# Performance work log

Hardware: AMD Instinct MI355X
Metric: run time of the kernel (lower is better)

The kernel has to match this reference:

```python
import jax, jax.numpy as jnp
import numpy as np

N_EMBED = 1024
HEAD_SIZE = 64
BLOCK_SIZE = 4096


def setup_inputs() -> dict:
    key = jax.random.key(0)
    ks = jax.random.split(key, 7)
    s = 1.0 / np.sqrt(N_EMBED)
    return {
        "batch_x": jax.random.normal(ks[0], (4, 4096, N_EMBED), dtype=jnp.float32),
        "Wk": jax.random.uniform(ks[1], (N_EMBED, HEAD_SIZE), jnp.float32, -s, s),
        "bk": jax.random.uniform(ks[2], (HEAD_SIZE,), jnp.float32, -s, s),
        "Wq": jax.random.uniform(ks[3], (N_EMBED, HEAD_SIZE), jnp.float32, -s, s),
        "bq": jax.random.uniform(ks[4], (HEAD_SIZE,), jnp.float32, -s, s),
        "Wv": jax.random.uniform(ks[5], (N_EMBED, HEAD_SIZE), jnp.float32, -s, s),
        "bv": jax.random.uniform(ks[6], (HEAD_SIZE,), jnp.float32, -s, s),
    }


def reference(batch_x, Wk, bk, Wq, bq, Wv, bv):
    # batch_x: [B, T, C]
    T = batch_x.shape[1]
    keys = batch_x @ Wk + bk      # [B, T, H]
    queries = batch_x @ Wq + bq   # [B, T, H]
    values = batch_x @ Wv + bv    # [B, T, H]
    scale = 1.0 / jnp.sqrt(jnp.asarray(HEAD_SIZE, batch_x.dtype))
    wei = jnp.einsum("bqh,bkh->bqk", queries, keys) * scale  # [B, T, T]
    causal = jnp.tril(jnp.ones((T, T), dtype=bool))
    wei = jnp.where(causal, wei, -jnp.inf)
    wei = jax.nn.softmax(wei, axis=-1)
    out = jnp.einsum("bqk,bkh->bqh", wei, values)  # [B, T, H]
    return out
```

## Files before the change

### kernel.cpp

```cpp
#include <hip/hip_runtime.h>


using bf16x8 = __attribute__((ext_vector_type(8))) short;
using bf16x4 = __attribute__((ext_vector_type(4))) short;
using f32x4  = __attribute__((ext_vector_type(4))) float;

#define QSCALE 0.1803368867f

__device__ __forceinline__ unsigned short f2bf(float f) {
  union { float f; unsigned int u; } v; v.f = f;
  unsigned int r = v.u + 0x7fffu + ((v.u >> 16) & 1u);
  return (unsigned short)(r >> 16);
}

__device__ __forceinline__ float fexp2(float x) {
#if __has_builtin(__builtin_amdgcn_exp2f)
  return __builtin_amdgcn_exp2f(x);
#else
  float r; asm("v_exp_f32 %0, %1" : "=v"(r) : "v"(x)); return r;
#endif
}

__device__ __forceinline__ void gl_lds16(const void* g, void* l) {
  __builtin_amdgcn_global_load_lds(
      (const __attribute__((address_space(1))) void*)g,
      (__attribute__((address_space(3))) void*)l, 16, 0, 0);
}

__device__ __forceinline__ f32x4 mfma16(bf16x4 a, bf16x4 b, f32x4 c) {
#if __has_builtin(__builtin_amdgcn_mfma_f32_16x16x16bf16_1k)
  return __builtin_amdgcn_mfma_f32_16x16x16bf16_1k(a, b, c, 0, 0, 0);
#else
  f32x4 d;
  asm volatile("v_mfma_f32_16x16x16_bf16 %0, %1, %2, %3"
               : "=v"(d) : "v"(a), "v"(b), "v"(c));
  return d;
#endif
}

__global__ __launch_bounds__(512) void proj6_kernel(
    const float* __restrict__ X,  const float* __restrict__ Wk,
    const float* __restrict__ Wq, const float* __restrict__ Wv,
    const float* __restrict__ bk, const float* __restrict__ bq,
    const float* __restrict__ bv, unsigned short* __restrict__ Kr,
    unsigned short* __restrict__ Qs, unsigned short* __restrict__ Vt) {
  __shared__ __align__(16) unsigned short Xl[32 * 72];
  __shared__ __align__(16) unsigned short Wl[192 * 72];
  const int tid = threadIdx.x;
  const int m0  = blockIdx.x * 32;
  const int w   = tid >> 6;
  const int mt  = w & 1;
  const int nh  = w >> 1;
  const int ln  = tid & 63;
  const int l15 = ln & 15;
  const int l4  = ln >> 4;
  const int wn  = tid & 63;
  const int wk8 = (tid >> 6) * 8;
  const int xr  = tid >> 4, xc = tid & 15;
  const f32x4 zero4 = {0.f, 0.f, 0.f, 0.f};

  f32x4 acc[3];
  #pragma unroll
  for (int i = 0; i < 3; ++i) acc[i] = zero4;

  float4 xp = *reinterpret_cast<const float4*>(X + (size_t)(m0 + xr) * 1024 + xc * 4);

  for (int kb = 0; kb < 16; ++kb) {
    __syncthreads();
    bf16x4 o;
    o[0] = (short)f2bf(xp.x); o[1] = (short)f2bf(xp.y);
    o[2] = (short)f2bf(xp.z); o[3] = (short)f2bf(xp.w);
    *reinterpret_cast<bf16x4*>(&Xl[xr * 72 + xc * 4]) = o;
    if (kb < 15) {
      xp = *reinterpret_cast<const float4*>(
          X + (size_t)(m0 + xr) * 1024 + (kb + 1) * 64 + xc * 4);
    }
    #pragma unroll
    for (int c = 0; c < 3; ++c) {
      const float* Wsrc = (c == 0) ? Wk : ((c == 1) ? Wq : Wv);
      bf16x8 w0;
      #pragma unroll
      for (int j = 0; j < 8; ++j)
        w0[j] = (short)f2bf(Wsrc[(size_t)(kb * 64 + wk8 + j) * 64 + wn]);
      *reinterpret_cast<bf16x8*>(&Wl[(c * 64 + wn) * 72 + wk8]) = w0;
    }
    __syncthreads();
    bf16x8 a0 = *reinterpret_cast<const bf16x8*>(&Xl[(mt * 16 + l15) * 72 + l4 * 8]);
    bf16x8 a1 = *reinterpret_cast<const bf16x8*>(&Xl[(mt * 16 + l15) * 72 + 32 + l4 * 8]);
    #pragma unroll
    for (int i = 0; i < 3; ++i) {
      int row = nh * 48 + i * 16 + l15;
      bf16x8 b0 = *reinterpret_cast<const bf16x8*>(&Wl[row * 72 + l4 * 8]);
      bf16x8 b1 = *reinterpret_cast<const bf16x8*>(&Wl[row * 72 + 32 + l4 * 8]);
      acc[i] = __builtin_amdgcn_mfma_f32_16x16x32_bf16(a0, b0, acc[i], 0, 0, 0);
      acc[i] = __builtin_amdgcn_mfma_f32_16x16x32_bf16(a1, b1, acc[i], 0, 0, 0);
    }
  }
  #pragma unroll
  for (int i = 0; i < 3; ++i) {
    int j = nh * 48 + i * 16 + l15;
    int mr0 = m0 + mt * 16 + l4 * 4;
    if (j < 64) {
      #pragma unroll
      for (int r = 0; r < 4; ++r)
        Kr[(size_t)(mr0 + r) * 64 + j] = f2bf(acc[i][r] + bk[j]);
    } else if (j < 128) {
      int jq = j - 64;
      #pragma unroll
      for (int r = 0; r < 4; ++r)
        Qs[(size_t)(mr0 + r) * 64 + jq] = f2bf((acc[i][r] + bq[jq]) * QSCALE);
    } else {
      int h = j - 128;
      int bb = mr0 >> 12, t0 = mr0 & 4095;
      ushort4 o;
      o.x = f2bf(acc[i][0] + bv[h]); o.y = f2bf(acc[i][1] + bv[h]);
      o.z = f2bf(acc[i][2] + bv[h]); o.w = f2bf(acc[i][3] + bv[h]);
      *reinterpret_cast<ushort4*>(&Vt[((size_t)(bb * 64 + h)) * 4096 + t0]) = o;
    }
  }
}

__global__ __launch_bounds__(512) void attn8_kernel(
    const unsigned short* __restrict__ Qs,
    const unsigned short* __restrict__ Kr,
    const unsigned short* __restrict__ Vt,
    float* __restrict__ out) {
  __shared__ __align__(16) char smem[98304];
  const int tid = threadIdx.x;
  const int w   = tid >> 6;
  const int ln  = tid & 63;
  const int l15 = ln & 15;
  const int l4  = ln >> 4;
  const int bid = blockIdx.x;
  const int pr  = bid >> 2;
  const int b   = bid & 3;
  const f32x4 zero4 = {0.f, 0.f, 0.f, 0.f};

  char* Kl = smem + w * 12288;
  char* Vl = Kl + 8192;

  const int kLane = (ln >> 3) * 128 + ((ln & 7) ^ (ln >> 3)) * 16;
  const int vLane = (ln >> 2) * 8192 + (((ln & 3) ^ ((ln >> 3) & 3))) * 16;
  const char* Kbase = (const char*)Kr + (size_t)b * 4096 * 128;
  const char* Vbase = (const char*)Vt + (size_t)b * 64 * 8192;

  auto phase = [&](int qt, bool entryBar) {
    if (entryBar) __syncthreads();
    const int qbase  = qt * 32;
    const int ntiles = qt + 1;

    const unsigned short* Q0 = Qs + ((size_t)b * 4096 + qbase + l15) * 64;
    const bf16x8 qa0 = *reinterpret_cast<const bf16x8*>(Q0 + l4 * 8);
    const bf16x8 qa1 = *reinterpret_cast<const bf16x8*>(Q0 + 32 + l4 * 8);
    const bf16x8 qb0 = *reinterpret_cast<const bf16x8*>(Q0 + 1024 + l4 * 8);
    const bf16x8 qb1 = *reinterpret_cast<const bf16x8*>(Q0 + 1024 + 32 + l4 * 8);

    f32x4 accA[4], accB[4];
    #pragma unroll
    for (int i = 0; i < 4; ++i) { accA[i] = zero4; accB[i] = zero4; }
    float mA = -1e30f, lA = 0.f, mB = -1e30f, lB = 0.f;

    auto stageK = [&](int buf, int t) {
      const char* src = Kbase + (size_t)t * 4096;
      char* dst = Kl + buf * 4096;
      #pragma unroll
      for (int c = 0; c < 4; ++c)
        gl_lds16(src + c * 1024 + kLane, dst + c * 1024 + ln * 16);
    };
    auto stageV = [&](int t) {
      const char* src = Vbase + (size_t)t * 64;
      #pragma unroll
      for (int c = 0; c < 4; ++c)
        gl_lds16(src + (size_t)c * 16 * 8192 + vLane, Vl + c * 1024 + ln * 16);
    };

    int cur = 0;
    if (w < ntiles) stageK(0, w);

    for (int t = w; t < ntiles; t += 8) {
      stageV(t);
      const bool hn = (t + 8 < ntiles);
      if (hn) stageK(cur ^ 1, t + 8);

      if (hn) asm volatile("s_waitcnt vmcnt(8)" ::: "memory");
      else    asm volatile("s_waitcnt vmcnt(4)" ::: "memory");
      __builtin_amdgcn_sched_barrier(0);

      f32x4 sA[2], sB[2];
      #pragma unroll
      for (int i = 0; i < 2; ++i) { sA[i] = zero4; sB[i] = zero4; }
      __builtin_amdgcn_s_setprio(1);
      #pragma unroll
      for (int nt = 0; nt < 2; ++nt) {
        const int krow = nt * 16 + l15;
        const unsigned short* kp =
            (const unsigned short*)(Kl + cur * 4096) + krow * 64;
        bf16x8 k0 = *reinterpret_cast<const bf16x8*>(kp + ((l4 ^ (krow & 7)) << 3));
        bf16x8 k1 = *reinterpret_cast<const bf16x8*>(kp + (((l4 + 4) ^ (krow & 7)) << 3));
        sA[nt] = __builtin_amdgcn_mfma_f32_16x16x32_bf16(k0, qa0, sA[nt], 0, 0, 0);
        sA[nt] = __builtin_amdgcn_mfma_f32_16x16x32_bf16(k1, qa1, sA[nt], 0, 0, 0);
        sB[nt] = __builtin_amdgcn_mfma_f32_16x16x32_bf16(k0, qb0, sB[nt], 0, 0, 0);
        sB[nt] = __builtin_amdgcn_mfma_f32_16x16x32_bf16(k1, qb1, sB[nt], 0, 0, 0);
      }
      __builtin_amdgcn_s_setprio(0);

      if (t == ntiles - 1) {
        const int qm = qbase + l15 - t * 32;
        #pragma unroll
        for (int nt = 0; nt < 2; ++nt)
          #pragma unroll
          for (int r = 0; r < 4; ++r) {
            int kvl = nt * 16 + 4 * l4 + r;
            if (kvl > qm)      sA[nt][r] = -1e30f;
            if (kvl > qm + 16) sB[nt][r] = -1e30f;
          }
      }

      bf16x4 paA[2], paB[2];
      {
        float x0 = fmaxf(fmaxf(sA[0][0], sA[0][1]), fmaxf(sA[0][2], sA[0][3]));
        float x1 = fmaxf(fmaxf(sA[1][0], sA[1][1]), fmaxf(sA[1][2], sA[1][3]));
        float xm = fmaxf(x0, x1);
        xm = fmaxf(xm, __shfl_xor(xm, 16));
        xm = fmaxf(xm, __shfl_xor(xm, 32));
        float mn = fmaxf(mA, xm);
        float cc = fexp2(mA - mn);
        mA = mn; lA *= cc;
        #pragma unroll
        for (int ht = 0; ht < 4; ++ht)
          #pragma unroll
          for (int r = 0; r < 4; ++r) accA[ht][r] *= cc;
        float sum = 0.f;
        #pragma unroll
        for (int nt = 0; nt < 2; ++nt) {
          #pragma unroll
          for (int r = 0; r < 4; ++r) {
            float p = fexp2(sA[nt][r] - mA);
            sA[nt][r] = p;
            paA[nt][r] = (short)f2bf(p);
          }
          sum += (sA[nt][0] + sA[nt][1]) + (sA[nt][2] + sA[nt][3]);
        }
        sum += __shfl_xor(sum, 16);
        sum += __shfl_xor(sum, 32);
        lA += sum;
      }
      {
        float x0 = fmaxf(fmaxf(sB[0][0], sB[0][1]), fmaxf(sB[0][2], sB[0][3]));
        float x1 = fmaxf(fmaxf(sB[1][0], sB[1][1]), fmaxf(sB[1][2], sB[1][3]));
        float xm = fmaxf(x0, x1);
        xm = fmaxf(xm, __shfl_xor(xm, 16));
        xm = fmaxf(xm, __shfl_xor(xm, 32));
        float mn = fmaxf(mB, xm);
        float cc = fexp2(mB - mn);
        mB = mn; lB *= cc;
        #pragma unroll
        for (int ht = 0; ht < 4; ++ht)
          #pragma unroll
          for (int r = 0; r < 4; ++r) accB[ht][r] *= cc;
        float sum = 0.f;
        #pragma unroll
        for (int nt = 0; nt < 2; ++nt) {
          #pragma unroll
          for (int r = 0; r < 4; ++r) {
            float p = fexp2(sB[nt][r] - mB);
            sB[nt][r] = p;
            paB[nt][r] = (short)f2bf(p);
          }
          sum += (sB[nt][0] + sB[nt][1]) + (sB[nt][2] + sB[nt][3]);
        }
        sum += __shfl_xor(sum, 16);
        sum += __shfl_xor(sum, 32);
        lB += sum;
      }

      if (hn) asm volatile("s_waitcnt vmcnt(4)" ::: "memory");
      else    asm volatile("s_waitcnt vmcnt(0)" ::: "memory");
      __builtin_amdgcn_sched_barrier(0);

      __builtin_amdgcn_s_setprio(1);
      #pragma unroll
      for (int nt = 0; nt < 2; ++nt) {
        #pragma unroll
        for (int ht = 0; ht < 4; ++ht) {
          const int vrow = ht * 16 + l15;
          const int g16 = (nt * 2 + (l4 >> 1)) ^ ((vrow >> 1) & 3);
          const char* vp = Vl + vrow * 64 + (g16 << 4) + ((l4 & 1) << 3);
          bf16x4 vf = *reinterpret_cast<const bf16x4*>(vp);
          accA[ht] = mfma16(vf, paA[nt], accA[ht]);
          accB[ht] = mfma16(vf, paB[nt], accB[ht]);
        }
      }
      __builtin_amdgcn_s_setprio(0);
      cur ^= 1;
    }

    __syncthreads();
    float* MO = (float*)smem;
    float* ML = (float*)(smem + 8 * 2 * 16 * 68 * 4);
    #pragma unroll
    for (int ht = 0; ht < 4; ++ht) {
      *reinterpret_cast<f32x4*>(&MO[((w * 2 + 0) * 16 + l15) * 68 + ht * 16 + 4 * l4]) = accA[ht];
      *reinterpret_cast<f32x4*>(&MO[((w * 2 + 1) * 16 + l15) * 68 + ht * 16 + 4 * l4]) = accB[ht];
    }
    if (l4 == 0) {
      ML[((w * 2 + 0) * 2 + 0) * 16 + l15] = mA;
      ML[((w * 2 + 0) * 2 + 1) * 16 + l15] = lA;
      ML[((w * 2 + 1) * 2 + 0) * 16 + l15] = mB;
      ML[((w * 2 + 1) * 2 + 1) * 16 + l15] = lB;
    }
    __syncthreads();
    {
      const int hf = tid >> 8;
      const int q  = (tid >> 4) & 15;
      const int hq = tid & 15;
      float mv[8], lv[8];
      float mM = -1e30f;
      #pragma unroll
      for (int p = 0; p < 8; ++p) {
        mv[p] = ML[((p * 2 + hf) * 2 + 0) * 16 + q];
        lv[p] = ML[((p * 2 + hf) * 2 + 1) * 16 + q];
        mM = fmaxf(mM, mv[p]);
      }
      float lT = 0.f, a[8];
      #pragma unroll
      for (int p = 0; p < 8; ++p) { a[p] = fexp2(mv[p] - mM); lT += lv[p] * a[p]; }
      float linv = 1.0f / lT;
      f32x4 o = zero4;
      #pragma unroll
      for (int p = 0; p < 8; ++p) {
        f32x4 v = *reinterpret_cast<const f32x4*>(
            &MO[((p * 2 + hf) * 16 + q) * 68 + hq * 4]);
        o[0] += v[0] * a[p]; o[1] += v[1] * a[p];
        o[2] += v[2] * a[p]; o[3] += v[3] * a[p];
      }
      float4 ov;
      ov.x = o[0] * linv; ov.y = o[1] * linv;
      ov.z = o[2] * linv; ov.w = o[3] * linv;
      *reinterpret_cast<float4*>(
          out + ((size_t)b * 4096 + qbase + hf * 16 + q) * 64 + hq * 4) = ov;
    }
  };

  phase(127 - pr, false);
  phase(pr, true);
}

template <bool WRITE_Q>
__global__ __launch_bounds__(256) void proj_kernel(
    const float* __restrict__ X,  const float* __restrict__ Wk,
    const float* __restrict__ Wq, const float* __restrict__ Wv,
    const float* __restrict__ bk, const float* __restrict__ bq,
    const float* __restrict__ bv, unsigned short* __restrict__ Kr,
    unsigned short* __restrict__ Qs, unsigned short* __restrict__ Vt) {
  constexpr int NT = WRITE_Q ? 12 : 8;
  constexpr int NC = NT / 4;
  __shared__ __align__(16) unsigned short Xl[64 * 72];
  __shared__ __align__(16) unsigned short Wl[NT * 16 * 72];
  const int tid = threadIdx.x;
  const int m0  = blockIdx.x * 64;
  const int w   = tid >> 6;
  const int ln  = tid & 63;
  const int l15 = ln & 15;
  const int l4  = ln >> 4;
  const f32x4 zero4 = {0.f, 0.f, 0.f, 0.f};
  f32x4 acc[NT];
  #pragma unroll
  for (int i = 0; i < NT; ++i) acc[i] = zero4;
  const int wn = tid & 63;
  const int wk = (tid >> 6) * 16;
  for (int kb = 0; kb < 16; ++kb) {
    __syncthreads();
    #pragma unroll
    for (int p = 0; p < 4; ++p) {
      int chunk = tid + p * 256;
      int r = chunk >> 4, c4 = chunk & 15;
      const float4 xv = *reinterpret_cast<const float4*>(
          X + (size_t)(m0 + r) * 1024 + kb * 64 + c4 * 4);
      bf16x4 o;
      o[0] = (short)f2bf(xv.x); o[1] = (short)f2bf(xv.y);
      o[2] = (short)f2bf(xv.z); o[3] = (short)f2bf(xv.w);
      *reinterpret_cast<bf16x4*>(&Xl[r * 72 + c4 * 4]) = o;
    }
    #pragma unroll
    for (int c = 0; c < NC; ++c) {
      const float* Wsrc = (c == 0) ? Wk : ((WRITE_Q && c == 1) ? Wq : Wv);
      bf16x8 w0, w1;
      #pragma unroll
      for (int j = 0; j < 8; ++j)
        w0[j] = (short)f2bf(Wsrc[(size_t)(kb * 64 + wk + j) * 64 + wn]);
      #pragma unroll
      for (int j = 0; j < 8; ++j)
        w1[j] = (short)f2bf(Wsrc[(size_t)(kb * 64 + wk + 8 + j) * 64 + wn]);
      *reinterpret_cast<bf16x8*>(&Wl[(c * 64 + wn) * 72 + wk])     = w0;
      *reinterpret_cast<bf16x8*>(&Wl[(c * 64 + wn) * 72 + wk + 8]) = w1;
    }
    __syncthreads();
    bf16x8 a0 = *reinterpret_cast<const bf16x8*>(&Xl[(w * 16 + l15) * 72 + l4 * 8]);
    bf16x8 a1 = *reinterpret_cast<const bf16x8*>(&Xl[(w * 16 + l15) * 72 + 32 + l4 * 8]);
    #pragma unroll
    for (int nt = 0; nt < NT; ++nt) {
      bf16x8 b0 = *reinterpret_cast<const bf16x8*>(&Wl[(nt * 16 + l15) * 72 + l4 * 8]);
      bf16x8 b1 = *reinterpret_cast<const bf16x8*>(&Wl[(nt * 16 + l15) * 72 + 32 + l4 * 8]);
      acc[nt] = __builtin_amdgcn_mfma_f32_16x16x32_bf16(a0, b0, acc[nt], 0, 0, 0);
      acc[nt] = __builtin_amdgcn_mfma_f32_16x16x32_bf16(a1, b1, acc[nt], 0, 0, 0);
    }
  }
  #pragma unroll
  for (int nt = 0; nt < NT; ++nt) {
    int j = nt * 16 + l15;
    #pragma unroll
    for (int r = 0; r < 4; ++r) {
      int m = m0 + w * 16 + l4 * 4 + r;
      float v = acc[nt][r];
      if (nt < 4) {
        Kr[(size_t)m * 64 + j] = f2bf(v + bk[j]);
      } else if (WRITE_Q && nt < 8) {
        Qs[(size_t)m * 64 + (j - 64)] = f2bf((v + bq[j - 64]) * QSCALE);
      } else {
        int h = j - (WRITE_Q ? 128 : 64);
        int bb = m >> 12, t = m & 4095;
        Vt[((size_t)(bb * 64 + h)) * 4096 + t] = f2bf(v + bv[h]);
      }
    }
  }
}

__global__ __launch_bounds__(256) void attnB_kernel(
    const unsigned short* __restrict__ Kr,
    const unsigned short* __restrict__ Vt,
    const float* __restrict__ X, const float* __restrict__ Wq,
    const float* __restrict__ bq, float* __restrict__ out) {
  __shared__ __align__(16) unsigned short Kl[64 * 72];
  __shared__ __align__(16) unsigned short Vl[64 * 72];
  __shared__ __align__(16) unsigned short Pl[4 * 16 * 72];
  const int tid = threadIdx.x;
  const int w   = tid >> 6;
  const int ln  = tid & 63;
  const int l15 = ln & 15;
  const int l4  = ln >> 4;
  const int b   = blockIdx.y;
  const int q0  = blockIdx.x * 64;
  const int qrow = q0 + w * 16;
  const f32x4 zero4 = {0.f, 0.f, 0.f, 0.f};
  unsigned short* Pw = &Pl[w * 16 * 72];
  f32x4 accq[4];
  #pragma unroll
  for (int i = 0; i < 4; ++i) accq[i] = zero4;
  const int wn = tid & 63;
  const int wk = (tid >> 6) * 16;
  for (int kb = 0; kb < 16; ++kb) {
    __syncthreads();
    #pragma unroll
    for (int p = 0; p < 4; ++p) {
      int chunk = tid + p * 256;
      int r = chunk >> 4, c4 = chunk & 15;
      const float4 xv = *reinterpret_cast<const float4*>(
          X + ((size_t)b * 4096 + q0 + r) * 1024 + kb * 64 + c4 * 4);
      bf16x4 o;
      o[0] = (short)f2bf(xv.x); o[1] = (short)f2bf(xv.y);
      o[2] = (short)f2bf(xv.z); o[3] = (short)f2bf(xv.w);
      *reinterpret_cast<bf16x4*>(&Kl[r * 72 + c4 * 4]) = o;
    }
    bf16x8 w0, w1;
    #pragma unroll
    for (int j = 0; j < 8; ++j)
      w0[j] = (short)f2bf(Wq[(size_t)(kb * 64 + wk + j) * 64 + wn]);
    #pragma unroll
    for (int j = 0; j < 8; ++j)
      w1[j] = (short)f2bf(Wq[(size_t)(kb * 64 + wk + 8 + j) * 64 + wn]);
    *reinterpret_cast<bf16x8*>(&Vl[wn * 72 + wk])     = w0;
    *reinterpret_cast<bf16x8*>(&Vl[wn * 72 + wk + 8]) = w1;
    __syncthreads();
    bf16x8 a0 = *reinterpret_cast<const bf16x8*>(&Kl[(w * 16 + l15) * 72 + l4 * 8]);
    bf16x8 a1 = *reinterpret_cast<const bf16x8*>(&Kl[(w * 16 + l15) * 72 + 32 + l4 * 8]);
    #pragma unroll
    for (int nt = 0; nt < 4; ++nt) {
      bf16x8 b0 = *reinterpret_cast<const bf16x8*>(&Vl[(nt * 16 + l15) * 72 + l4 * 8]);
      bf16x8 b1 = *reinterpret_cast<const bf16x8*>(&Vl[(nt * 16 + l15) * 72 + 32 + l4 * 8]);
      accq[nt] = __builtin_amdgcn_mfma_f32_16x16x32_bf16(a0, b0, accq[nt], 0, 0, 0);
      accq[nt] = __builtin_amdgcn_mfma_f32_16x16x32_bf16(a1, b1, accq[nt], 0, 0, 0);
    }
  }
  #pragma unroll
  for (int nt = 0; nt < 4; ++nt) {
    int h = nt * 16 + l15;
    #pragma unroll
    for (int r = 0; r < 4; ++r)
      Pw[(l4 * 4 + r) * 72 + h] = f2bf((accq[nt][r] + bq[h]) * 0.125f);
  }
  asm volatile("s_waitcnt lgkmcnt(0)" ::: "memory");
  __builtin_amdgcn_sched_barrier(0);
  bf16x8 qa0 = *reinterpret_cast<const bf16x8*>(&Pw[l15 * 72 + l4 * 8]);
  bf16x8 qa1 = *reinterpret_cast<const bf16x8*>(&Pw[l15 * 72 + 32 + l4 * 8]);
  f32x4 acco[4];
  #pragma unroll
  for (int i = 0; i < 4; ++i) acco[i] = zero4;
  float mrow[4] = {-1e30f, -1e30f, -1e30f, -1e30f};
  float lrow[4] = {0.f, 0.f, 0.f, 0.f};
  const int ktmax = blockIdx.x;
  for (int kt = 0; kt <= ktmax; ++kt) {
    const int kv0 = kt * 64;
    __syncthreads();
    #pragma unroll
    for (int p = 0; p < 2; ++p) {
      int chunk = tid + p * 256;
      int r = chunk >> 3, c8 = chunk & 7;
      *reinterpret_cast<bf16x8*>(&Kl[r * 72 + c8 * 8]) =
          *reinterpret_cast<const bf16x8*>(Kr + ((size_t)b * 4096 + kv0 + r) * 64 + c8 * 8);
      *reinterpret_cast<bf16x8*>(&Vl[r * 72 + c8 * 8]) =
          *reinterpret_cast<const bf16x8*>(Vt + ((size_t)b * 64 + r) * 4096 + kv0 + c8 * 8);
    }
    __syncthreads();
    f32x4 s[4];
    #pragma unroll
    for (int i = 0; i < 4; ++i) s[i] = zero4;
    #pragma unroll
    for (int nt = 0; nt < 4; ++nt) {
      bf16x8 k0 = *reinterpret_cast<const bf16x8*>(&Kl[(nt * 16 + l15) * 72 + l4 * 8]);
      bf16x8 k1 = *reinterpret_cast<const bf16x8*>(&Kl[(nt * 16 + l15) * 72 + 32 + l4 * 8]);
      s[nt] = __builtin_amdgcn_mfma_f32_16x16x32_bf16(qa0, k0, s[nt], 0, 0, 0);
      s[nt] = __builtin_amdgcn_mfma_f32_16x16x32_bf16(qa1, k1, s[nt], 0, 0, 0);
    }
    if (kt == ktmax) {
      #pragma unroll
      for (int nt = 0; nt < 4; ++nt) {
        int kv_g = kv0 + nt * 16 + l15;
        #pragma unroll
        for (int r = 0; r < 4; ++r) {
          int q_g = qrow + l4 * 4 + r;
          if (kv_g > q_g) s[nt][r] = -1e30f;
        }
      }
    }
    #pragma unroll
    for (int r = 0; r < 4; ++r) {
      float t = fmaxf(fmaxf(s[0][r], s[1][r]), fmaxf(s[2][r], s[3][r]));
      t = fmaxf(t, __shfl_xor(t, 1));
      t = fmaxf(t, __shfl_xor(t, 2));
      t = fmaxf(t, __shfl_xor(t, 4));
      t = fmaxf(t, __shfl_xor(t, 8));
      float mnew = fmaxf(mrow[r], t);
      float cc = __expf(mrow[r] - mnew);
      mrow[r] = mnew;
      lrow[r] *= cc;
      acco[0][r] *= cc; acco[1][r] *= cc; acco[2][r] *= cc; acco[3][r] *= cc;
    }
    #pragma unroll
    for (int nt = 0; nt < 4; ++nt) {
      #pragma unroll
      for (int r = 0; r < 4; ++r) {
        float p = __expf(s[nt][r] - mrow[r]);
        s[nt][r] = p;
        Pw[(l4 * 4 + r) * 72 + nt * 16 + l15] = f2bf(p);
      }
    }
    #pragma unroll
    for (int r = 0; r < 4; ++r) {
      float t = s[0][r] + s[1][r] + s[2][r] + s[3][r];
      t += __shfl_xor(t, 1);
      t += __shfl_xor(t, 2);
      t += __shfl_xor(t, 4);
      t += __shfl_xor(t, 8);
      lrow[r] += t;
    }
    asm volatile("s_waitcnt lgkmcnt(0)" ::: "memory");
    __builtin_amdgcn_sched_barrier(0);
    #pragma unroll
    for (int ks = 0; ks < 2; ++ks) {
      bf16x8 pa = *reinterpret_cast<const bf16x8*>(&Pw[l15 * 72 + ks * 32 + l4 * 8]);
      #pragma unroll
      for (int ht = 0; ht < 4; ++ht) {
        bf16x8 vf = *reinterpret_cast<const bf16x8*>(&Vl[(ht * 16 + l15) * 72 + ks * 32 + l4 * 8]);
        acco[ht] = __builtin_amdgcn_mfma_f32_16x16x32_bf16(pa, vf, acco[ht], 0, 0, 0);
      }
    }
  }
  float* ob = out + ((size_t)b * 4096 + qrow) * 64;
  #pragma unroll
  for (int ht = 0; ht < 4; ++ht) {
    #pragma unroll
    for (int r = 0; r < 4; ++r) {
      ob[(l4 * 4 + r) * 64 + ht * 16 + l15] = acco[ht][r] / lrow[r];
    }
  }
}

extern "C" void kernel_launch(void* const* d_in, const int* in_sizes, int n_in,
                              void* d_out, int out_size, void* d_ws, size_t ws_size,
                              hipStream_t stream) {
  const float* X  = (const float*)d_in[0];
  const float* Wk = (const float*)d_in[1];
  const float* bk = (const float*)d_in[2];
  const float* Wq = (const float*)d_in[3];
  const float* bq = (const float*)d_in[4];
  const float* Wv = (const float*)d_in[5];
  const float* bv = (const float*)d_in[6];
  float* out = (float*)d_out;

  char* ws = (char*)d_ws;
  const size_t SZ = 2097152;
  unsigned short* Kr = (unsigned short*)(ws);
  unsigned short* Vt = (unsigned short*)(ws + SZ);

  if (ws_size >= 3 * SZ) {
    unsigned short* Qs = (unsigned short*)(ws + 2 * SZ);
    proj6_kernel<<<512, 512, 0, stream>>>(X, Wk, Wq, Wv, bk, bq, bv, Kr, Qs, Vt);
    attn8_kernel<<<256, 512, 0, stream>>>(Qs, Kr, Vt, out);
  } else {
    proj_kernel<false><<<256, 256, 0, stream>>>(X, Wk, Wq, Wv, bk, bq, bv, Kr, nullptr, Vt);
    attnB_kernel<<<dim3(64, 4), 256, 0, stream>>>(Kr, Vt, X, Wq, bq, out);
  }
}
```

Before: 61.31 us.

## Pre-transpose weights to bf16 and double-buffer projection loads via direct-to-LDS

Adds a small pre-kernel that converts Wk/Wq/Wv to a transposed bf16 layout once per call. This removes the strided fp32 weight gathers and conversions that every projection block used to repeat. The projection kernel now stages X (as fp32) and the weights straight into XOR-swizzled, double-buffered LDS using global_load_lds, converting X to bf16 at read time. That overlaps the next tile's loads with the MFMAs and halves the barriers. The cost is an extra kernel launch, double the LDS footprint, and fp32 X in LDS. If the workspace is too small it falls back to borrowing the output buffer for scratch.

```diff
diff --git a/kernel.cpp b/kernel.cpp
--- a/kernel.cpp
+++ b/kernel.cpp
@@ -38,14 +38,26 @@
 #endif
 }
 
-__global__ __launch_bounds__(512) void proj6_kernel(
-    const float* __restrict__ X,  const float* __restrict__ Wk,
-    const float* __restrict__ Wq, const float* __restrict__ Wv,
+__global__ __launch_bounds__(256) void prep_w_kernel(
+    const float* __restrict__ Wk, const float* __restrict__ Wq,
+    const float* __restrict__ Wv, unsigned short* __restrict__ Wt) {
+  int j = blockIdx.x;
+  const float* src = (j < 64) ? Wk : ((j < 128) ? Wq : Wv);
+  int jj = j & 63;
+  #pragma unroll
+  for (int p = 0; p < 4; ++p) {
+    int k = threadIdx.x + p * 256;
+    Wt[j * 1024 + k] = f2bf(src[k * 64 + jj]);
+  }
+}
+
+__global__ __launch_bounds__(512) void proj8_kernel(
+    const float* __restrict__ X, const unsigned short* __restrict__ Wt,
     const float* __restrict__ bk, const float* __restrict__ bq,
     const float* __restrict__ bv, unsigned short* __restrict__ Kr,
     unsigned short* __restrict__ Qs, unsigned short* __restrict__ Vt) {
-  __shared__ __align__(16) unsigned short Xl[32 * 72];
-  __shared__ __align__(16) unsigned short Wl[192 * 72];
+  __shared__ __align__(16) float          Xl[2][32 * 64];
+  __shared__ __align__(16) unsigned short Wl[2][192 * 64];
   const int tid = threadIdx.x;
   const int m0  = blockIdx.x * 32;
   const int w   = tid >> 6;
@@ -54,48 +66,66 @@
   const int ln  = tid & 63;
   const int l15 = ln & 15;
   const int l4  = ln >> 4;
-  const int wn  = tid & 63;
-  const int wk8 = (tid >> 6) * 8;
-  const int xr  = tid >> 4, xc = tid & 15;
   const f32x4 zero4 = {0.f, 0.f, 0.f, 0.f};
 
+  const int xr = tid >> 4, xc = tid & 15;
+  const size_t xsrcLane = (size_t)(m0 + xr) * 4096 + ((xc ^ (xr & 7)) << 4);
+  const char* Xb = (const char*)X;
+  const char* Wb = (const char*)Wt;
+
   f32x4 acc[3];
   #pragma unroll
   for (int i = 0; i < 3; ++i) acc[i] = zero4;
 
-  float4 xp = *reinterpret_cast<const float4*>(X + (size_t)(m0 + xr) * 1024 + xc * 4);
-
+  auto stageX = [&](int buf, int kb) {
+    gl_lds16(Xb + xsrcLane + kb * 256, (char*)&Xl[buf][0] + tid * 16);
+  };
+  auto stageW = [&](int buf, int kb) {
+    #pragma unroll
+    for (int s = 0; s < 3; ++s) {
+      int g = tid + s * 512;
+      int row = g >> 3, gc = g & 7;
+      gl_lds16(Wb + (size_t)row * 2048 + kb * 128 + ((gc ^ (row & 7)) << 4),
+               (char*)&Wl[buf][0] + g * 16);
+    }
+  };
+
+  stageX(0, 0);
+  stageW(0, 0);
+  asm volatile("s_waitcnt vmcnt(0)" ::: "memory");
+  __syncthreads();
+
+  const int rr = mt * 16 + l15;
+  const int rs7 = rr & 7;
   for (int kb = 0; kb < 16; ++kb) {
-    __syncthreads();
-    bf16x4 o;
-    o[0] = (short)f2bf(xp.x); o[1] = (short)f2bf(xp.y);
-    o[2] = (short)f2bf(xp.z); o[3] = (short)f2bf(xp.w);
-    *reinterpret_cast<bf16x4*>(&Xl[xr * 72 + xc * 4]) = o;
-    if (kb < 15) {
-      xp = *reinterpret_cast<const float4*>(
-          X + (size_t)(m0 + xr) * 1024 + (kb + 1) * 64 + xc * 4);
-    }
-    #pragma unroll
-    for (int c = 0; c < 3; ++c) {
-      const float* Wsrc = (c == 0) ? Wk : ((c == 1) ? Wq : Wv);
-      bf16x8 w0;
-      #pragma unroll
-      for (int j = 0; j < 8; ++j)
-        w0[j] = (short)f2bf(Wsrc[(size_t)(kb * 64 + wk8 + j) * 64 + wn]);
-      *reinterpret_cast<bf16x8*>(&Wl[(c * 64 + wn) * 72 + wk8]) = w0;
-    }
-    __syncthreads();
-    bf16x8 a0 = *reinterpret_cast<const bf16x8*>(&Xl[(mt * 16 + l15) * 72 + l4 * 8]);
-    bf16x8 a1 = *reinterpret_cast<const bf16x8*>(&Xl[(mt * 16 + l15) * 72 + 32 + l4 * 8]);
+    const int buf = kb & 1;
+    if (kb + 1 < 16) {
+      stageX(buf ^ 1, kb + 1);
+      stageW(buf ^ 1, kb + 1);
+    }
+    const float* xp = &Xl[buf][0] + rr * 64;
+    f32x4 xa0 = *reinterpret_cast<const f32x4*>(xp + (((2 * l4)     ^ rs7) << 2));
+    f32x4 xa1 = *reinterpret_cast<const f32x4*>(xp + (((2 * l4 + 1) ^ rs7) << 2));
+    f32x4 xb0 = *reinterpret_cast<const f32x4*>(xp + (((8 + 2 * l4) ^ rs7) << 2));
+    f32x4 xb1 = *reinterpret_cast<const f32x4*>(xp + (((9 + 2 * l4) ^ rs7) << 2));
+    bf16x8 a0, a1;
+    #pragma unroll
+    for (int i = 0; i < 4; ++i) {
+      a0[i] = (short)f2bf(xa0[i]); a0[4 + i] = (short)f2bf(xa1[i]);
+      a1[i] = (short)f2bf(xb0[i]); a1[4 + i] = (short)f2bf(xb1[i]);
+    }
     #pragma unroll
     for (int i = 0; i < 3; ++i) {
-      int row = nh * 48 + i * 16 + l15;
-      bf16x8 b0 = *reinterpret_cast<const bf16x8*>(&Wl[row * 72 + l4 * 8]);
-      bf16x8 b1 = *reinterpret_cast<const bf16x8*>(&Wl[row * 72 + 32 + l4 * 8]);
+      const int row = nh * 48 + i * 16 + l15;
+      const unsigned short* wp = &Wl[buf][0] + row * 64;
+      bf16x8 b0 = *reinterpret_cast<const bf16x8*>(wp + ((l4       ^ (row & 7)) << 3));
+      bf16x8 b1 = *reinterpret_cast<const bf16x8*>(wp + (((4 + l4) ^ (row & 7)) << 3));
       acc[i] = __builtin_amdgcn_mfma_f32_16x16x32_bf16(a0, b0, acc[i], 0, 0, 0);
       acc[i] = __builtin_amdgcn_mfma_f32_16x16x32_bf16(a1, b1, acc[i], 0, 0, 0);
     }
-  }
+    if (kb + 1 < 16) __syncthreads();
+  }
+
   #pragma unroll
   for (int i = 0; i < 3; ++i) {
     int j = nh * 48 + i * 16 + l15;
@@ -600,12 +630,17 @@
 
   char* ws = (char*)d_ws;
   const size_t SZ = 2097152;
+  const size_t WT = 393216;
   unsigned short* Kr = (unsigned short*)(ws);
   unsigned short* Vt = (unsigned short*)(ws + SZ);
 
   if (ws_size >= 3 * SZ) {
     unsigned short* Qs = (unsigned short*)(ws + 2 * SZ);
-    proj6_kernel<<<512, 512, 0, stream>>>(X, Wk, Wq, Wv, bk, bq, bv, Kr, Qs, Vt);
+    unsigned short* Wt = (ws_size >= 3 * SZ + WT)
+                             ? (unsigned short*)(ws + 3 * SZ)
+                             : (unsigned short*)d_out;
+    prep_w_kernel<<<192, 256, 0, stream>>>(Wk, Wq, Wv, Wt);
+    proj8_kernel<<<512, 512, 0, stream>>>(X, Wt, bk, bq, bv, Kr, Qs, Vt);
     attn8_kernel<<<256, 512, 0, stream>>>(Qs, Kr, Vt, out);
   } else {
     proj_kernel<false><<<256, 256, 0, stream>>>(X, Wk, Wq, Wv, bk, bq, bv, Kr, nullptr, Vt);
```

Result: faster. 58.19 us, median of 2 (-5.1%).
